# Optimization experiments

Measured on AMD Instinct MI355X. Metric: run time of the kernel, lower is better.

Reference implementation:

```python
import jax, jax.numpy as jnp
import numpy as np

B, N, D = 8, 256, 42   # batch, natoms, nFeatures
H1, H2 = 64, 32        # dmirror_FC hidden sizes


def setup_inputs() -> dict:
    key = jax.random.key(0)
    ks = jax.random.split(key, 8)
    s1, s2, s3 = (1.0 / np.sqrt(D)), (1.0 / np.sqrt(H1)), (1.0 / np.sqrt(H2))
    return {
        "image": jax.random.normal(ks[0], (B, N, D), dtype=jnp.float32),
        "dfeat": jax.random.normal(ks[1], (B, N, N, D, 3), dtype=jnp.float32),
        "W1": jax.random.normal(ks[2], (D, H1), dtype=jnp.float32) * s1,
        "b1": jax.random.normal(ks[3], (H1,), dtype=jnp.float32) * s1,
        "W2": jax.random.normal(ks[4], (H1, H2), dtype=jnp.float32) * s2,
        "b2": jax.random.normal(ks[5], (H2,), dtype=jnp.float32) * s2,
        "W3": jax.random.normal(ks[6], (H2, 1), dtype=jnp.float32) * s3,
        "b3": jax.random.normal(ks[7], (1,), dtype=jnp.float32) * s3,
    }


def reference(image, dfeat, W1, b1, W2, b2, W3, b3):
    # Per-atom mirrored MLP (dmirror_FC, softplus activation, d(softplus)=sigmoid),
    # fully vectorized over (batch, atom) instead of nested Python loops.
    z1 = image @ W1 + b1                 # [B,N,H1]
    a1 = jax.nn.softplus(z1)
    z2 = a1 @ W2 + b2                    # [B,N,H2]
    a2 = jax.nn.softplus(z2)
    Ei = (a2 @ W3 + b3)[..., 0]          # [B,N]
    Etot = jnp.sum(Ei, axis=1)           # [B]

    # Analytic mirrored backward: dEi/dFeat via chain rule
    g2 = jax.nn.sigmoid(z2) * W3[:, 0]   # [B,N,H2]
    g1 = jax.nn.sigmoid(z1) * (g2 @ W2.T)  # [B,N,H1]
    dEi_dFeat = g1 @ W1.T                # [B,N,D]

    # Force[b,i,:] = dEtot_dFeat[b] @ dfeat[b,i].reshape(N*D,3)
    Force = jnp.einsum('bjf,bijfc->bic', dEi_dFeat, dfeat)  # [B,N,3]
    return Etot, Force
```

## Files before the change

kernel.cpp:

```cpp
#include <hip/hip_runtime.h>

#define BATCH 8
#define NATOM 256
#define DF    42
#define H1    64
#define H2    32

typedef float f32x4 __attribute__((ext_vector_type(4)));

__device__ __forceinline__ float softplus_f(float z) {
  return fmaxf(z, 0.f) + log1pf(expf(-fabsf(z)));
}

__global__ __launch_bounds__(256) void k1_mlp(
    const float* __restrict__ image,
    const float* __restrict__ W1, const float* __restrict__ b1,
    const float* __restrict__ W2, const float* __restrict__ b2,
    const float* __restrict__ W3, const float* __restrict__ b3,
    float* __restrict__ dG, float* __restrict__ Ei_ws) {
  __shared__ float sW1 [DF*H1];
  __shared__ float sW1T[H1*DF];
  __shared__ float sW2 [H1*H2];
  __shared__ float sW2T[H2*H1];
  __shared__ float sW3[H2], sb1[H1], sb2[H2];

  const int tid = threadIdx.x;
  for (int idx = tid; idx < DF*H1; idx += 256) {
    float w = W1[idx];
    sW1[idx] = w;
    sW1T[(idx & (H1-1))*DF + (idx >> 6)] = w;
  }
  for (int idx = tid; idx < H1*H2; idx += 256) {
    float w = W2[idx];
    sW2[idx] = w;
    sW2T[(idx & (H2-1))*H1 + (idx >> 5)] = w;
  }
  if (tid < H2)                    { sW3[tid] = W3[tid]; sb2[tid] = b2[tid]; }
  else if (tid >= 64 && tid < 128) { sb1[tid-64] = b1[tid-64]; }
  __syncthreads();

  const int lane = tid & 63;
  const int atom = blockIdx.x * 4 + (tid >> 6);

  float xv = (lane < DF) ? image[atom*DF + lane] : 0.f;

  float z1 = sb1[lane];
  #pragma unroll
  for (int d = 0; d < DF; ++d)
    z1 = fmaf(__shfl(xv, d), sW1[d*H1 + lane], z1);
  float a1 = softplus_f(z1);

  const int h2l = lane & (H2-1);
  float z2 = sb2[h2l];
  #pragma unroll
  for (int h = 0; h < H1; ++h)
    z2 = fmaf(__shfl(a1, h), sW2[h*H2 + h2l], z2);
  float a2 = softplus_f(z2);

  float w3  = sW3[h2l];
  float eip = a2 * w3;
  #pragma unroll
  for (int off = 16; off; off >>= 1) eip += __shfl_xor(eip, off);
  float g2 = (1.f - expf(-a2)) * w3;

  float t1 = 0.f;
  #pragma unroll
  for (int h2 = 0; h2 < H2; ++h2)
    t1 = fmaf(__shfl(g2, h2), sW2T[h2*H1 + lane], t1);
  float g1 = (1.f - expf(-a1)) * t1;

  const int dl = (lane < DF) ? lane : 0;
  float s = 0.f;
  #pragma unroll
  for (int h = 0; h < H1; ++h)
    s = fmaf(__shfl(g1, h), sW1T[h*DF + dl], s);

  if (lane < DF) dG[atom*DF + lane] = s;
  if (lane == 0) Ei_ws[atom] = eip + b3[0];
}

__global__ __launch_bounds__(512, 4) void k2_force(
    const float* __restrict__ dfeat,
    const float* __restrict__ dG,
    const float* __restrict__ Ei_ws,
    float* __restrict__ out) {
  __shared__ f32x4 dgL[NATOM*DF/4];
  __shared__ float red[4][8][3];
  __shared__ float ered[4];

  const int tid = threadIdx.x;
  const int blk = blockIdx.x;
  const int b = blk >> 6;

  const f32x4* __restrict__ dgg = (const f32x4*)(dG + b*(NATOM*DF));
  #pragma unroll
  for (int m = 0; m < 5; ++m) dgL[tid + m*512] = dgg[tid + m*512];
  if (tid < 128) dgL[tid + 2560] = dgg[tid + 2560];

  if ((blk & 63) == 0 && tid < 256) {
    float e = Ei_ws[b*NATOM + tid];
    #pragma unroll
    for (int off = 32; off; off >>= 1) e += __shfl_down(e, off);
    if ((tid & 63) == 0) ered[tid >> 6] = e;
  }
  __syncthreads();

  const int wv = tid >> 6;
  for (int r = 0; r < 4; ++r) {
    const int R = blk*4 + r;
    const f32x4* __restrict__ p4 = (const f32x4*)(dfeat + (size_t)R * (NATOM*DF*3));

    float ax = 0.f, ay = 0.f, az = 0.f;
    #pragma unroll
    for (int m = 0; m < 5; ++m) {
      const int g = tid + m*512;
      f32x4 v0 = p4[3*g + 0];
      f32x4 v1 = p4[3*g + 1];
      f32x4 v2 = p4[3*g + 2];
      f32x4 gg = dgL[g];
      ax += gg.x*v0.x + gg.y*v0.w + gg.z*v1.z + gg.w*v2.y;
      ay += gg.x*v0.y + gg.y*v1.x + gg.z*v1.w + gg.w*v2.z;
      az += gg.x*v0.z + gg.y*v1.y + gg.z*v2.x + gg.w*v2.w;
    }
    if (tid < 128) {
      const int g = tid + 2560;
      f32x4 v0 = p4[3*g + 0];
      f32x4 v1 = p4[3*g + 1];
      f32x4 v2 = p4[3*g + 2];
      f32x4 gg = dgL[g];
      ax += gg.x*v0.x + gg.y*v0.w + gg.z*v1.z + gg.w*v2.y;
      ay += gg.x*v0.y + gg.y*v1.x + gg.z*v1.w + gg.w*v2.z;
      az += gg.x*v0.z + gg.y*v1.y + gg.z*v2.x + gg.w*v2.w;
    }

    #pragma unroll
    for (int off = 32; off; off >>= 1) {
      ax += __shfl_down(ax, off);
      ay += __shfl_down(ay, off);
      az += __shfl_down(az, off);
    }
    if ((tid & 63) == 0) { red[r][wv][0] = ax; red[r][wv][1] = ay; red[r][wv][2] = az; }
  }

  __syncthreads();
  if (tid < 12) {
    const int r = tid >> 2 == 0 ? tid / 3 : tid / 3;
    const int c = tid - (tid/3)*3;
    float s = 0.f;
    #pragma unroll
    for (int w = 0; w < 8; ++w) s += red[tid/3][w][c];
    out[BATCH + (size_t)(blk*4 + tid/3)*3 + c] = s;
  }
  if ((blk & 63) == 0 && tid == 12)
    out[b] = ered[0] + ered[1] + ered[2] + ered[3];
}

extern "C" void kernel_launch(void* const* d_in, const int* in_sizes, int n_in,
                              void* d_out, int out_size, void* d_ws, size_t ws_size,
                              hipStream_t stream) {
  const float* image = (const float*)d_in[0];
  const float* dfeat = (const float*)d_in[1];
  const float* W1    = (const float*)d_in[2];
  const float* b1    = (const float*)d_in[3];
  const float* W2    = (const float*)d_in[4];
  const float* b2    = (const float*)d_in[5];
  const float* W3    = (const float*)d_in[6];
  const float* b3    = (const float*)d_in[7];
  float* out = (float*)d_out;

  float* dG = (float*)d_ws;
  float* Ei = dG + BATCH*NATOM*DF;

  k1_mlp<<<BATCH*NATOM/4, 256, 0, stream>>>(image, W1, b1, W2, b2, W3, b3, dG, Ei);
  k2_force<<<BATCH*NATOM/4, 512, 0, stream>>>(dfeat, dG, Ei, out);
}
```

Measured before the change: 57.37 us.

## Coalesce dfeat loads in force kernel with rotating component accumulators

The force kernel now has each thread read consecutive float4s of dfeat (stride 512 float4 per step) instead of three strided float4s per feature group. Each float4 spans mixed feature/component positions, so the matching dG values are fetched as scalars from LDS and three accumulators rotate roles, with a per-thread remap before the wave reduction. This is meant to give fully contiguous per-instruction global loads for the dominant dfeat stream, at the cost of extra scalar LDS reads and select logic.

New measurement: 57.31 us. Within noise of the previous version (-0.1%).

```diff
diff --git a/kernel.cpp b/kernel.cpp
--- a/kernel.cpp
+++ b/kernel.cpp
@@ -84,7 +84,7 @@
     const float* __restrict__ dG,
     const float* __restrict__ Ei_ws,
     float* __restrict__ out) {
-  __shared__ f32x4 dgL[NATOM*DF/4];
+  __shared__ float dgLf[NATOM*DF];
   __shared__ float red[4][8][3];
   __shared__ float ered[4];
 
@@ -93,9 +93,10 @@
   const int b = blk >> 6;
 
   const f32x4* __restrict__ dgg = (const f32x4*)(dG + b*(NATOM*DF));
+  f32x4* dgv = (f32x4*)dgLf;
   #pragma unroll
-  for (int m = 0; m < 5; ++m) dgL[tid + m*512] = dgg[tid + m*512];
-  if (tid < 128) dgL[tid + 2560] = dgg[tid + 2560];
+  for (int m = 0; m < 5; ++m) dgv[tid + m*512] = dgg[tid + m*512];
+  if (tid < 128) dgv[tid + 2560] = dgg[tid + 2560];
 
   if ((blk & 63) == 0 && tid < 256) {
     float e = Ei_ws[b*NATOM + tid];
@@ -105,51 +106,60 @@
   }
   __syncthreads();
 
-  const int wv = tid >> 6;
+  const int wv  = tid >> 6;
+  const int f0i = (4*tid)/3;
+  const int rqi = tid - (tid/3)*3;
+
   for (int r = 0; r < 4; ++r) {
-    const int R = blk*4 + r;
-    const f32x4* __restrict__ p4 = (const f32x4*)(dfeat + (size_t)R * (NATOM*DF*3));
+    const f32x4* __restrict__ p4 =
+        (const f32x4*)(dfeat + (size_t)(blk*4 + r) * (NATOM*DF*3)) + tid;
 
-    float ax = 0.f, ay = 0.f, az = 0.f;
+    float a0 = 0.f, a1 = 0.f, a2 = 0.f;
+    int f0 = f0i, rq = rqi;
+
+    auto iter = [&](int m, float& pa, float& pb, float& pc) {
+      f32x4 v = p4[m*512];
+      float gLo = dgLf[f0];
+      float gHi = dgLf[f0+1];
+      float gm1 = (rq < 2) ? gLo : gHi;
+      float gm2 = (rq < 1) ? gLo : gHi;
+      pa = fmaf(v.x, gLo, pa);
+      pb = fmaf(v.y, gm1, pb);
+      pc = fmaf(v.z, gm2, pc);
+      pa = fmaf(v.w, gHi, pa);
+      f0 += 682 + (rq >= 1 ? 1 : 0);
+      rq = (rq >= 1) ? rq - 1 : 2;
+    };
+
     #pragma unroll
-    for (int m = 0; m < 5; ++m) {
-      const int g = tid + m*512;
-      f32x4 v0 = p4[3*g + 0];
-      f32x4 v1 = p4[3*g + 1];
-      f32x4 v2 = p4[3*g + 2];
-      f32x4 gg = dgL[g];
-      ax += gg.x*v0.x + gg.y*v0.w + gg.z*v1.z + gg.w*v2.y;
-      ay += gg.x*v0.y + gg.y*v1.x + gg.z*v1.w + gg.w*v2.z;
-      az += gg.x*v0.z + gg.y*v1.y + gg.z*v2.x + gg.w*v2.w;
+    for (int mm = 0; mm < 5; ++mm) {
+      iter(3*mm + 0, a0, a1, a2);
+      iter(3*mm + 1, a2, a0, a1);
+      iter(3*mm + 2, a1, a2, a0);
     }
-    if (tid < 128) {
-      const int g = tid + 2560;
-      f32x4 v0 = p4[3*g + 0];
-      f32x4 v1 = p4[3*g + 1];
-      f32x4 v2 = p4[3*g + 2];
-      f32x4 gg = dgL[g];
-      ax += gg.x*v0.x + gg.y*v0.w + gg.z*v1.z + gg.w*v2.y;
-      ay += gg.x*v0.y + gg.y*v1.x + gg.z*v1.w + gg.w*v2.z;
-      az += gg.x*v0.z + gg.y*v1.y + gg.z*v2.x + gg.w*v2.w;
-    }
+    if (tid < 384) iter(15, a0, a1, a2);
+
+    float tx = (rqi == 0) ? a0 : (rqi == 1) ? a2 : a1;
+    float ty = (rqi == 0) ? a1 : (rqi == 1) ? a0 : a2;
+    float tz = (rqi == 0) ? a2 : (rqi == 1) ? a1 : a0;
 
     #pragma unroll
     for (int off = 32; off; off >>= 1) {
-      ax += __shfl_down(ax, off);
-      ay += __shfl_down(ay, off);
-      az += __shfl_down(az, off);
+      tx += __shfl_down(tx, off);
+      ty += __shfl_down(ty, off);
+      tz += __shfl_down(tz, off);
     }
-    if ((tid & 63) == 0) { red[r][wv][0] = ax; red[r][wv][1] = ay; red[r][wv][2] = az; }
+    if ((tid & 63) == 0) { red[r][wv][0] = tx; red[r][wv][1] = ty; red[r][wv][2] = tz; }
   }
 
   __syncthreads();
   if (tid < 12) {
-    const int r = tid >> 2 == 0 ? tid / 3 : tid / 3;
-    const int c = tid - (tid/3)*3;
+    const int rr = tid / 3;
+    const int c  = tid - rr*3;
     float s = 0.f;
     #pragma unroll
-    for (int w = 0; w < 8; ++w) s += red[tid/3][w][c];
-    out[BATCH + (size_t)(blk*4 + tid/3)*3 + c] = s;
+    for (int w = 0; w < 8; ++w) s += red[rr][w][c];
+    out[BATCH + (size_t)(blk*4 + rr)*3 + c] = s;
   }
   if ((blk & 63) == 0 && tid == 12)
     out[b] = ered[0] + ered[1] + ered[2] + ered[3];
```
